# Optimization experiments

Measured on AMD Instinct MI355X. Metric: run time of the kernel, lower is better.

The kernel has to match this reference:

```python
import jax, jax.numpy as jnp
import numpy as np

H = 1024   # hidden_dim
NH = 16    # num_heads
HD = H // NH  # head_dim = 64
B, S = 2, 2048
LN_EPS = 1e-5


def setup_inputs() -> dict:
    key = jax.random.key(0)
    ks = jax.random.split(key, 5)
    scale = 1.0 / np.sqrt(H)  # xavier-ish scale for stability
    return {
        "x": jax.random.normal(ks[0], (B, S, H), dtype=jnp.float32),
        "Wq": jax.random.normal(ks[1], (H, H), dtype=jnp.float32) * scale,
        "bq": jnp.zeros((H,), jnp.float32),
        "Wk": jax.random.normal(ks[2], (H, H), dtype=jnp.float32) * scale,
        "bk": jnp.zeros((H,), jnp.float32),
        "Wv": jax.random.normal(ks[3], (H, H), dtype=jnp.float32) * scale,
        "bv": jnp.zeros((H,), jnp.float32),
        "Wo": jax.random.normal(ks[4], (H, H), dtype=jnp.float32) * scale,
        "bo": jnp.zeros((H,), jnp.float32),
        "ln_gamma": jnp.ones((H,), jnp.float32),
        "ln_beta": jnp.zeros((H,), jnp.float32),
    }


def reference(x, Wq, bq, Wk, bk, Wv, bv, Wo, bo, ln_gamma, ln_beta):
    b, s, _ = x.shape
    # QKV projections, split heads: (b, nh, s, hd)
    def split_heads(t):
        return t.reshape(b, s, NH, HD).transpose(0, 2, 1, 3)
    Q = split_heads(x @ Wq + bq)
    K = split_heads(x @ Wk + bk)
    V = split_heads(x @ Wv + bv)
    # scaled dot-product with clamp (mask=None path)
    scores = jnp.einsum('bhqd,bhkd->bhqk', Q, K) / np.sqrt(HD).astype(np.float32)
    scores = jnp.clip(scores, -10000.0, 10000.0)
    attn = jax.nn.softmax(scores, axis=-1)
    # dropout is identity in eval mode
    ctx = jnp.einsum('bhqk,bhkd->bhqd', attn, V)
    ctx = ctx.transpose(0, 2, 1, 3).reshape(b, s, H)
    out = ctx @ Wo + bo
    # residual + LayerNorm
    y = out + x
    mu = jnp.mean(y, axis=-1, keepdims=True)
    var = jnp.mean(jnp.square(y - mu), axis=-1, keepdims=True)
    y = (y - mu) * jax.lax.rsqrt(var + LN_EPS)
    return y * ln_gamma + ln_beta
```

## Files before the change

### kernel.cpp

```cpp
#include <hip/hip_runtime.h>

typedef unsigned short u16;
typedef __attribute__((ext_vector_type(8))) short shortx8;
typedef __attribute__((ext_vector_type(4))) float floatx4;

#define GLD16(gp, lp) __builtin_amdgcn_global_load_lds( \
    (__attribute__((address_space(1))) void*)(gp), \
    (__attribute__((address_space(3))) void*)(lp), 16, 0, 0)

__device__ __forceinline__ u16 f2bf(float f) {
  union { float f; unsigned u; } v; v.f = f;
  unsigned r = v.u + 0x7FFFu + ((v.u >> 16) & 1u);
  return (u16)(r >> 16);
}

__device__ __forceinline__ u16 f2bf_fast(float f) {
  union { float f; unsigned u; } v; v.f = f;
  return (u16)((v.u + 0x8000u) >> 16);
}

__global__ __launch_bounds__(256) void cast_x_kernel(const float* __restrict__ x,
                                                     u16* __restrict__ xb, int n4) {
  int i = blockIdx.x * 256 + threadIdx.x;
  if (i < n4) {
    float4 v = ((const float4*)x)[i];
    ushort4 o;
    o.x = f2bf(v.x); o.y = f2bf(v.y); o.z = f2bf(v.z); o.w = f2bf(v.w);
    ((ushort4*)xb)[i] = o;
  }
}

__global__ __launch_bounds__(256) void transpose_cast_w(const float* __restrict__ Wq,
                                                        const float* __restrict__ Wk,
                                                        const float* __restrict__ Wv,
                                                        const float* __restrict__ Wo,
                                                        u16* __restrict__ Wt) {
  __shared__ u16 tile[32][33];
  int mat = blockIdx.z;
  const float* W = (mat == 0) ? Wq : (mat == 1) ? Wk : (mat == 2) ? Wv : Wo;
  u16* dst = Wt + (size_t)mat * 1024 * 1024;
  int n0 = blockIdx.x * 32, k0 = blockIdx.y * 32;
  int tx = threadIdx.x, ty = threadIdx.y;
  for (int i = 0; i < 4; ++i)
    tile[ty + i * 8][tx] = f2bf(W[(size_t)(k0 + ty + i * 8) * 1024 + n0 + tx]);
  __syncthreads();
  for (int i = 0; i < 4; ++i)
    dst[(size_t)(n0 + ty + i * 8) * 1024 + k0 + tx] = tile[tx][ty + i * 8];
}

__device__ __forceinline__ void gemm_tile_core(const u16* __restrict__ A,
                                               const u16* __restrict__ Bt,
                                               int m0, int n0,
                                               u16* As, u16* Bs,
                                               floatx4 (&acc)[4][4]) {
  const int tid = threadIdx.x;
  const int wave = tid >> 6, lane = tid & 63;
  const int lrow = lane >> 4, lcol = lane & 15;
  const int wm = wave >> 1, wn = wave & 1;

  for (int mi = 0; mi < 4; ++mi)
    for (int ni = 0; ni < 4; ++ni)
      acc[mi][ni] = (floatx4){0.f, 0.f, 0.f, 0.f};

  const u16* ap[4];
  const u16* bp[4];
  for (int l = 0; l < 4; ++l) {
    int g = (l * 4 + wave) * 64 + lane;
    int r = g >> 3, c = g & 7;
    int cc = (c ^ (r & 7)) * 8;
    ap[l] = A + (size_t)(m0 + r) * 1024 + cc;
    bp[l] = Bt + (size_t)(n0 + r) * 1024 + cc;
  }

  for (int k0 = 0; k0 < 1024; k0 += 64) {
    __syncthreads();
    for (int l = 0; l < 4; ++l) {
      GLD16(ap[l], As + (l * 4 + wave) * 512);
      GLD16(bp[l], Bs + (l * 4 + wave) * 512);
      ap[l] += 64; bp[l] += 64;
    }
    __syncthreads();
    for (int kk = 0; kk < 2; ++kk) {
      shortx8 af[4], bf[4];
      for (int mi = 0; mi < 4; ++mi) {
        int row = wm * 64 + mi * 16 + lcol;
        int gr = (kk * 4 + lrow) ^ (row & 7);
        af[mi] = *(const shortx8*)&As[row * 64 + gr * 8];
      }
      for (int ni = 0; ni < 4; ++ni) {
        int row = wn * 64 + ni * 16 + lcol;
        int gr = (kk * 4 + lrow) ^ (row & 7);
        bf[ni] = *(const shortx8*)&Bs[row * 64 + gr * 8];
      }
      for (int mi = 0; mi < 4; ++mi)
        for (int ni = 0; ni < 4; ++ni)
          acc[mi][ni] = __builtin_amdgcn_mfma_f32_16x16x32_bf16(af[mi], bf[ni], acc[mi][ni], 0, 0, 0);
    }
  }
}

__global__ __launch_bounds__(256) void qkv_gemm(const u16* __restrict__ xb,
                                                const u16* __restrict__ Wt,
                                                const float* __restrict__ bq,
                                                const float* __restrict__ bk,
                                                const float* __restrict__ bv,
                                                u16* __restrict__ Qh,
                                                u16* __restrict__ Kh,
                                                u16* __restrict__ Vth) {
  __shared__ u16 As[128 * 64];
  __shared__ u16 Bs[128 * 64];
  int m0 = blockIdx.x * 128;
  int mat = blockIdx.y >> 3;
  int n0 = (blockIdx.y & 7) * 128;
  floatx4 acc[4][4];
  gemm_tile_core(xb, Wt + (size_t)mat * 1024 * 1024, m0, n0, As, Bs, acc);

  const float* bias = (mat == 0) ? bq : (mat == 1) ? bk : bv;
  const int tid = threadIdx.x;
  const int wave = tid >> 6, lane = tid & 63;
  const int lrow = lane >> 4, lcol = lane & 15;
  const int wm = wave >> 1, wn = wave & 1;

  for (int mi = 0; mi < 4; ++mi) {
    int mbase = m0 + wm * 64 + mi * 16 + lrow * 4;
    for (int ni = 0; ni < 4; ++ni) {
      int n = n0 + wn * 64 + ni * 16 + lcol;
      float bval = bias[n];
      int h = n >> 6, d = n & 63;
      if (mat < 2) {
        u16* dst = (mat == 0) ? Qh : Kh;
        for (int r = 0; r < 4; ++r) {
          int m = mbase + r;
          int bb = m >> 11, s = m & 2047;
          dst[((size_t)(bb * 16 + h) * 2048 + s) * 64 + d] = f2bf(acc[mi][ni][r] + bval);
        }
      } else {
        int bb = mbase >> 11, s = mbase & 2047;
        ushort4 pk;
        pk.x = f2bf(acc[mi][ni][0] + bval);
        pk.y = f2bf(acc[mi][ni][1] + bval);
        pk.z = f2bf(acc[mi][ni][2] + bval);
        pk.w = f2bf(acc[mi][ni][3] + bval);
        *(ushort4*)&Vth[((size_t)(bb * 16 + h) * 64 + d) * 2048 + s] = pk;
      }
    }
  }
}

__global__ __launch_bounds__(256) void out_gemm(const u16* __restrict__ ctx,
                                                const u16* __restrict__ Wot,
                                                const float* __restrict__ bo,
                                                float* __restrict__ aout) {
  __shared__ u16 As[128 * 64];
  __shared__ u16 Bs[128 * 64];
  int m0 = blockIdx.x * 128;
  int n0 = blockIdx.y * 128;
  floatx4 acc[4][4];
  gemm_tile_core(ctx, Wot, m0, n0, As, Bs, acc);

  const int tid = threadIdx.x;
  const int wave = tid >> 6, lane = tid & 63;
  const int lrow = lane >> 4, lcol = lane & 15;
  const int wm = wave >> 1, wn = wave & 1;
  for (int mi = 0; mi < 4; ++mi) {
    int mbase = m0 + wm * 64 + mi * 16 + lrow * 4;
    for (int ni = 0; ni < 4; ++ni) {
      int n = n0 + wn * 64 + ni * 16 + lcol;
      float bval = bo[n];
      for (int r = 0; r < 4; ++r)
        aout[(size_t)(mbase + r) * 1024 + n] = acc[mi][ni][r] + bval;
    }
  }
}

__global__ __launch_bounds__(256) void attn_kernel(const u16* __restrict__ Qh,
                                                   const u16* __restrict__ Kh,
                                                   const u16* __restrict__ Vth,
                                                   u16* __restrict__ ctx) {
  __shared__ u16 Qs[128 * 64];
  __shared__ u16 Ks[2][64 * 64];
  __shared__ u16 Vs[2][64 * 64];
  __shared__ u16 Ps[128 * 64];

  int bh = blockIdx.y;
  int b = bh >> 4, h = bh & 15;
  int q0 = blockIdx.x * 128;
  int tid = threadIdx.x;
  int wave = tid >> 6, lane = tid & 63;
  int lrow = lane >> 4, lcol = lane & 15;

  const u16* Qg = Qh + ((size_t)bh * 2048 + q0) * 64;
  for (int l = 0; l < 4; ++l) {
    int g = (l * 4 + wave) * 64 + lane;
    int r = g >> 3, c = g & 7;
    GLD16(Qg + r * 64 + ((c ^ (r & 7)) * 8), Qs + (l * 4 + wave) * 512);
  }

  const u16* Kbase = Kh + (size_t)bh * 2048 * 64;
  const u16* Vbase = Vth + (size_t)bh * 64 * 2048;

  int gr0[2], gc0[2];
  for (int l = 0; l < 2; ++l) {
    int gg = (l * 4 + wave) * 64 + lane;
    int r = gg >> 3, c = gg & 7;
    gr0[l] = r;
    gc0[l] = (c ^ (r & 7)) * 8;
  }
  for (int l = 0; l < 2; ++l) {
    GLD16(Kbase + (size_t)gr0[l] * 64 + gc0[l], Ks[0] + (l * 4 + wave) * 512);
    GLD16(Vbase + (size_t)gr0[l] * 2048 + gc0[l], Vs[0] + (l * 4 + wave) * 512);
  }
  __syncthreads();

  shortx8 qf[2][2];
  for (int kk = 0; kk < 2; ++kk)
    for (int qt = 0; qt < 2; ++qt) {
      int row = wave * 32 + qt * 16 + lcol;
      int gr = (kk * 4 + lrow) ^ (row & 7);
      qf[kk][qt] = *(const shortx8*)&Qs[row * 64 + gr * 8];
    }

  floatx4 o[2][4];
  float rs[2][4];
  for (int qt = 0; qt < 2; ++qt) {
    for (int dt = 0; dt < 4; ++dt) o[qt][dt] = (floatx4){0.f, 0.f, 0.f, 0.f};
    for (int r = 0; r < 4; ++r) rs[qt][r] = 0.f;
  }

  const float C1 = 0.18033688011f;

  for (int i = 0; i < 32; ++i) {
    int cur = i & 1;
    if (i < 31) {
      int kc = (i + 1) * 64;
      for (int l = 0; l < 2; ++l) {
        GLD16(Kbase + (size_t)(kc + gr0[l]) * 64 + gc0[l], Ks[cur ^ 1] + (l * 4 + wave) * 512);
        GLD16(Vbase + (size_t)gr0[l] * 2048 + kc + gc0[l], Vs[cur ^ 1] + (l * 4 + wave) * 512);
      }
    }

    floatx4 sc[2][4];
    for (int qt = 0; qt < 2; ++qt)
      for (int kt = 0; kt < 4; ++kt)
        sc[qt][kt] = (floatx4){0.f, 0.f, 0.f, 0.f};
    for (int kk = 0; kk < 2; ++kk) {
      shortx8 kf[4];
      for (int kt = 0; kt < 4; ++kt) {
        int row = kt * 16 + lcol;
        int gr = (kk * 4 + lrow) ^ (row & 7);
        kf[kt] = *(const shortx8*)&Ks[cur][row * 64 + gr * 8];
      }
      for (int qt = 0; qt < 2; ++qt)
        for (int kt = 0; kt < 4; ++kt)
          sc[qt][kt] = __builtin_amdgcn_mfma_f32_16x16x32_bf16(qf[kk][qt], kf[kt], sc[qt][kt], 0, 0, 0);
    }

    for (int qt = 0; qt < 2; ++qt)
      for (int kt = 0; kt < 4; ++kt)
        for (int r = 0; r < 4; ++r) {
          float p = __builtin_amdgcn_exp2f(sc[qt][kt][r] * C1);
          sc[qt][kt][r] = p;
          rs[qt][r] += p;
        }

    for (int qt = 0; qt < 2; ++qt)
      for (int kt = 0; kt < 4; ++kt)
        for (int r = 0; r < 4; ++r) {
          int row = wave * 32 + qt * 16 + lrow * 4 + r;
          int col = kt * 16 + lcol;
          Ps[row * 64 + (((col >> 3) ^ (row & 7)) * 8) + (col & 7)] = f2bf_fast(sc[qt][kt][r]);
        }

    for (int kk = 0; kk < 2; ++kk) {
      shortx8 pf[2];
      for (int qt = 0; qt < 2; ++qt) {
        int row = wave * 32 + qt * 16 + lcol;
        int gr = (kk * 4 + lrow) ^ (row & 7);
        pf[qt] = *(const shortx8*)&Ps[row * 64 + gr * 8];
      }
      for (int dt = 0; dt < 4; ++dt) {
        int row = dt * 16 + lcol;
        int gr = (kk * 4 + lrow) ^ (row & 7);
        shortx8 vf = *(const shortx8*)&Vs[cur][row * 64 + gr * 8];
        for (int qt = 0; qt < 2; ++qt)
          o[qt][dt] = __builtin_amdgcn_mfma_f32_16x16x32_bf16(pf[qt], vf, o[qt][dt], 0, 0, 0);
      }
    }
    __syncthreads();
  }

  for (int qt = 0; qt < 2; ++qt)
    for (int r = 0; r < 4; ++r) {
      float l = rs[qt][r];
      l += __shfl_xor(l, 1, 64);
      l += __shfl_xor(l, 2, 64);
      l += __shfl_xor(l, 4, 64);
      l += __shfl_xor(l, 8, 64);
      float inv = 1.0f / l;
      int s = q0 + wave * 32 + qt * 16 + lrow * 4 + r;
      for (int dt = 0; dt < 4; ++dt) {
        int d = dt * 16 + lcol;
        ctx[(size_t)(b * 2048 + s) * 1024 + h * 64 + d] = f2bf(o[qt][dt][r] * inv);
      }
    }
}

__global__ __launch_bounds__(256) void ln_kernel(const float* __restrict__ aout,
                                                 const float* __restrict__ x,
                                                 const float* __restrict__ gamma,
                                                 const float* __restrict__ beta,
                                                 float* __restrict__ out) {
  int row = blockIdx.x;
  int t = threadIdx.x;
  const float4* a4 = (const float4*)(aout + (size_t)row * 1024);
  const float4* x4 = (const float4*)(x + (size_t)row * 1024);
  float4 v = a4[t];
  float4 xv = x4[t];
  v.x += xv.x; v.y += xv.y; v.z += xv.z; v.w += xv.w;
  float s = v.x + v.y + v.z + v.w;
  float s2 = v.x * v.x + v.y * v.y + v.z * v.z + v.w * v.w;
  for (int off = 1; off < 64; off <<= 1) {
    s += __shfl_xor(s, off, 64);
    s2 += __shfl_xor(s2, off, 64);
  }
  __shared__ float red[8];
  int wave = t >> 6, lane = t & 63;
  if (lane == 0) { red[wave] = s; red[4 + wave] = s2; }
  __syncthreads();
  s = red[0] + red[1] + red[2] + red[3];
  s2 = red[4] + red[5] + red[6] + red[7];
  float mu = s * (1.0f / 1024.0f);
  float var = s2 * (1.0f / 1024.0f) - mu * mu;
  float rstd = rsqrtf(var + 1e-5f);
  float4 g = ((const float4*)gamma)[t];
  float4 be = ((const float4*)beta)[t];
  float4 y;
  y.x = (v.x - mu) * rstd * g.x + be.x;
  y.y = (v.y - mu) * rstd * g.y + be.y;
  y.z = (v.z - mu) * rstd * g.z + be.z;
  y.w = (v.w - mu) * rstd * g.w + be.w;
  ((float4*)(out + (size_t)row * 1024))[t] = y;
}

extern "C" void kernel_launch(void* const* d_in, const int* in_sizes, int n_in,
                              void* d_out, int out_size, void* d_ws, size_t ws_size,
                              hipStream_t stream) {
  const float* x     = (const float*)d_in[0];
  const float* Wq    = (const float*)d_in[1];
  const float* bq    = (const float*)d_in[2];
  const float* Wk    = (const float*)d_in[3];
  const float* bk    = (const float*)d_in[4];
  const float* Wv    = (const float*)d_in[5];
  const float* bv    = (const float*)d_in[6];
  const float* Wo    = (const float*)d_in[7];
  const float* bo    = (const float*)d_in[8];
  const float* gamma = (const float*)d_in[9];
  const float* beta  = (const float*)d_in[10];
  float* out = (float*)d_out;

  char* ws = (char*)d_ws;
  u16* xb   = (u16*)(ws);
  u16* Wt   = (u16*)(ws + ((size_t)8 << 20));
  u16* Qh   = (u16*)(ws + ((size_t)16 << 20));
  u16* Kh   = (u16*)(ws + ((size_t)24 << 20));
  u16* Vth  = (u16*)(ws + ((size_t)32 << 20));
  u16* ctx  = (u16*)(ws + ((size_t)40 << 20));
  float* aout = (float*)(ws + ((size_t)48 << 20));

  cast_x_kernel<<<4096, 256, 0, stream>>>(x, xb, 1048576);
  transpose_cast_w<<<dim3(32, 32, 4), dim3(32, 8), 0, stream>>>(Wq, Wk, Wv, Wo, Wt);
  qkv_gemm<<<dim3(32, 24), 256, 0, stream>>>(xb, Wt, bq, bk, bv, Qh, Kh, Vth);
  attn_kernel<<<dim3(16, 32), 256, 0, stream>>>(Qh, Kh, Vth, ctx);
  out_gemm<<<dim3(32, 8), 256, 0, stream>>>(ctx, Wt + (size_t)3 * 1024 * 1024, bo, aout);
  ln_kernel<<<4096, 256, 0, stream>>>(aout, x, gamma, beta, out);
}
```

Baseline: 232.3 us.

## Transpose attention MFMA operands, fold softmax scale into Q, pack P stores

Swaps the MFMA operand order so the score and output accumulators come out transposed, with each lane holding four consecutive key or head-dim values for one query row. This lets P be written to shared memory as packed 8-byte stores, lets the context be written as ushort4, and cuts the row-sum reduction to two shuffles. The softmax scale is folded into Q inside the QKV GEMM epilogue, and the Q and P shared buffers are merged to reduce LDS use, which needs an extra barrier after Q is loaded. Pre-scaling Q before the bf16 rounding slightly changes numerics.

```diff
diff --git a/kernel.cpp b/kernel.cpp
--- a/kernel.cpp
+++ b/kernel.cpp
@@ -3,6 +3,7 @@
 typedef unsigned short u16;
 typedef __attribute__((ext_vector_type(8))) short shortx8;
 typedef __attribute__((ext_vector_type(4))) float floatx4;
+typedef __attribute__((ext_vector_type(2))) unsigned uintx2;
 
 #define GLD16(gp, lp) __builtin_amdgcn_global_load_lds( \
     (__attribute__((address_space(1))) void*)(gp), \
@@ -14,9 +15,9 @@
   return (u16)(r >> 16);
 }
 
-__device__ __forceinline__ u16 f2bf_fast(float f) {
+__device__ __forceinline__ unsigned f2bf_u32(float f) {
   union { float f; unsigned u; } v; v.f = f;
-  return (u16)((v.u + 0x8000u) >> 16);
+  return (v.u + 0x8000u) >> 16;
 }
 
 __global__ __launch_bounds__(256) void cast_x_kernel(const float* __restrict__ x,
@@ -120,6 +121,7 @@
   const int wave = tid >> 6, lane = tid & 63;
   const int lrow = lane >> 4, lcol = lane & 15;
   const int wm = wave >> 1, wn = wave & 1;
+  const float qscale = 0.18033688011f;
 
   for (int mi = 0; mi < 4; ++mi) {
     int mbase = m0 + wm * 64 + mi * 16 + lrow * 4;
@@ -129,10 +131,11 @@
       int h = n >> 6, d = n & 63;
       if (mat < 2) {
         u16* dst = (mat == 0) ? Qh : Kh;
+        float sc = (mat == 0) ? qscale : 1.0f;
         for (int r = 0; r < 4; ++r) {
           int m = mbase + r;
           int bb = m >> 11, s = m & 2047;
-          dst[((size_t)(bb * 16 + h) * 2048 + s) * 64 + d] = f2bf(acc[mi][ni][r] + bval);
+          dst[((size_t)(bb * 16 + h) * 2048 + s) * 64 + d] = f2bf((acc[mi][ni][r] + bval) * sc);
         }
       } else {
         int bb = mbase >> 11, s = mbase & 2047;
@@ -177,10 +180,9 @@
                                                    const u16* __restrict__ Kh,
                                                    const u16* __restrict__ Vth,
                                                    u16* __restrict__ ctx) {
-  __shared__ u16 Qs[128 * 64];
+  __shared__ u16 QPs[128 * 64];
   __shared__ u16 Ks[2][64 * 64];
   __shared__ u16 Vs[2][64 * 64];
-  __shared__ u16 Ps[128 * 64];
 
   int bh = blockIdx.y;
   int b = bh >> 4, h = bh & 15;
@@ -193,7 +195,7 @@
   for (int l = 0; l < 4; ++l) {
     int g = (l * 4 + wave) * 64 + lane;
     int r = g >> 3, c = g & 7;
-    GLD16(Qg + r * 64 + ((c ^ (r & 7)) * 8), Qs + (l * 4 + wave) * 512);
+    GLD16(Qg + r * 64 + ((c ^ (r & 7)) * 8), QPs + (l * 4 + wave) * 512);
   }
 
   const u16* Kbase = Kh + (size_t)bh * 2048 * 64;
@@ -217,17 +219,16 @@
     for (int qt = 0; qt < 2; ++qt) {
       int row = wave * 32 + qt * 16 + lcol;
       int gr = (kk * 4 + lrow) ^ (row & 7);
-      qf[kk][qt] = *(const shortx8*)&Qs[row * 64 + gr * 8];
-    }
+      qf[kk][qt] = *(const shortx8*)&QPs[row * 64 + gr * 8];
+    }
+  __syncthreads();
 
   floatx4 o[2][4];
-  float rs[2][4];
+  float rs[2];
   for (int qt = 0; qt < 2; ++qt) {
     for (int dt = 0; dt < 4; ++dt) o[qt][dt] = (floatx4){0.f, 0.f, 0.f, 0.f};
-    for (int r = 0; r < 4; ++r) rs[qt][r] = 0.f;
-  }
-
-  const float C1 = 0.18033688011f;
+    rs[qt] = 0.f;
+  }
 
   for (int i = 0; i < 32; ++i) {
     int cur = i & 1;
@@ -252,57 +253,63 @@
       }
       for (int qt = 0; qt < 2; ++qt)
         for (int kt = 0; kt < 4; ++kt)
-          sc[qt][kt] = __builtin_amdgcn_mfma_f32_16x16x32_bf16(qf[kk][qt], kf[kt], sc[qt][kt], 0, 0, 0);
+          sc[qt][kt] = __builtin_amdgcn_mfma_f32_16x16x32_bf16(kf[kt], qf[kk][qt], sc[qt][kt], 0, 0, 0);
     }
 
     for (int qt = 0; qt < 2; ++qt)
       for (int kt = 0; kt < 4; ++kt)
         for (int r = 0; r < 4; ++r) {
-          float p = __builtin_amdgcn_exp2f(sc[qt][kt][r] * C1);
+          float p = __builtin_amdgcn_exp2f(sc[qt][kt][r]);
           sc[qt][kt][r] = p;
-          rs[qt][r] += p;
+          rs[qt] += p;
         }
 
-    for (int qt = 0; qt < 2; ++qt)
-      for (int kt = 0; kt < 4; ++kt)
-        for (int r = 0; r < 4; ++r) {
-          int row = wave * 32 + qt * 16 + lrow * 4 + r;
-          int col = kt * 16 + lcol;
-          Ps[row * 64 + (((col >> 3) ^ (row & 7)) * 8) + (col & 7)] = f2bf_fast(sc[qt][kt][r]);
-        }
+    for (int qt = 0; qt < 2; ++qt) {
+      int row = wave * 32 + qt * 16 + lcol;
+      for (int kt = 0; kt < 4; ++kt) {
+        int g = kt * 2 + (lrow >> 1);
+        int addr = row * 64 + ((g ^ (row & 7)) * 8) + (lrow & 1) * 4;
+        uintx2 pk;
+        pk.x = f2bf_u32(sc[qt][kt][0]) | (f2bf_u32(sc[qt][kt][1]) << 16);
+        pk.y = f2bf_u32(sc[qt][kt][2]) | (f2bf_u32(sc[qt][kt][3]) << 16);
+        *(uintx2*)&QPs[addr] = pk;
+      }
+    }
 
     for (int kk = 0; kk < 2; ++kk) {
       shortx8 pf[2];
       for (int qt = 0; qt < 2; ++qt) {
         int row = wave * 32 + qt * 16 + lcol;
         int gr = (kk * 4 + lrow) ^ (row & 7);
-        pf[qt] = *(const shortx8*)&Ps[row * 64 + gr * 8];
+        pf[qt] = *(const shortx8*)&QPs[row * 64 + gr * 8];
       }
       for (int dt = 0; dt < 4; ++dt) {
         int row = dt * 16 + lcol;
         int gr = (kk * 4 + lrow) ^ (row & 7);
         shortx8 vf = *(const shortx8*)&Vs[cur][row * 64 + gr * 8];
         for (int qt = 0; qt < 2; ++qt)
-          o[qt][dt] = __builtin_amdgcn_mfma_f32_16x16x32_bf16(pf[qt], vf, o[qt][dt], 0, 0, 0);
+          o[qt][dt] = __builtin_amdgcn_mfma_f32_16x16x32_bf16(vf, pf[qt], o[qt][dt], 0, 0, 0);
       }
     }
     __syncthreads();
   }
 
-  for (int qt = 0; qt < 2; ++qt)
-    for (int r = 0; r < 4; ++r) {
-      float l = rs[qt][r];
-      l += __shfl_xor(l, 1, 64);
-      l += __shfl_xor(l, 2, 64);
-      l += __shfl_xor(l, 4, 64);
-      l += __shfl_xor(l, 8, 64);
-      float inv = 1.0f / l;
-      int s = q0 + wave * 32 + qt * 16 + lrow * 4 + r;
-      for (int dt = 0; dt < 4; ++dt) {
-        int d = dt * 16 + lcol;
-        ctx[(size_t)(b * 2048 + s) * 1024 + h * 64 + d] = f2bf(o[qt][dt][r] * inv);
-      }
-    }
+  for (int qt = 0; qt < 2; ++qt) {
+    float l = rs[qt];
+    l += __shfl_xor(l, 16, 64);
+    l += __shfl_xor(l, 32, 64);
+    float inv = 1.0f / l;
+    int s = q0 + wave * 32 + qt * 16 + lcol;
+    u16* dst = ctx + (size_t)(b * 2048 + s) * 1024 + h * 64 + lrow * 4;
+    for (int dt = 0; dt < 4; ++dt) {
+      ushort4 pk;
+      pk.x = f2bf(o[qt][dt][0] * inv);
+      pk.y = f2bf(o[qt][dt][1] * inv);
+      pk.z = f2bf(o[qt][dt][2] * inv);
+      pk.w = f2bf(o[qt][dt][3] * inv);
+      *(ushort4*)(dst + dt * 16) = pk;
+    }
+  }
 }
 
 __global__ __launch_bounds__(256) void ln_kernel(const float* __restrict__ aout,
```

New measurement: 221.2 us. -4.8%, faster.
